# Kernel optimization log

Measured on AMD Instinct MI355X. Metric: run time of the kernel, lower is better.

Reference implementation:

```python
import jax, jax.numpy as jnp
import numpy as np

H = 1024
D = 512


def _cummax(z):
    # CumMax = cumsum(softmax(z, -1), -1)
    return jnp.cumsum(jax.nn.softmax(z, axis=-1), axis=-1)


def _onlstm_layer(x, h0, c0, W, b):
    # x: [T, M, Din]; W: [Din+H, 6H] fused (order: i, f, g, o, ftilde, itilde)
    def step(carry, xt):
        h, c = carry
        z = jnp.concatenate([xt, h], axis=-1) @ W + b  # [M, 6H]
        zi, zf, zg, zo, zft, zit = jnp.split(z, 6, axis=-1)
        f_t = jax.nn.sigmoid(zf)
        i_t = jax.nn.sigmoid(zi)
        o_t = jax.nn.sigmoid(zo)
        c_hat = jnp.tanh(zg)
        f_til = _cummax(zft)
        i_til = 1.0 - _cummax(zit)
        omega = f_til * i_til
        f_hat = f_t * omega + (f_til - omega)
        i_hat = i_t * omega + (i_til - omega)
        c = f_hat * c + i_hat * c_hat
        h = o_t * jnp.tanh(c)
        return (h, c), h

    (h_n, c_n), all_h = jax.lax.scan(step, (h0, c0), x)
    return all_h, h_n, c_n


def setup_inputs() -> dict:
    key = jax.random.key(0)
    k = jax.random.split(key, 5)
    T, M = 256, 64
    inp = {
        "input_": jax.random.normal(k[0], (T, M, D), dtype=jnp.float32),
        # fused gate weights: layer0 in = D+H, layer1 in = H+H; out = 6H
        "W0": jax.random.normal(k[1], (D + H, 6 * H), dtype=jnp.float32) / np.sqrt(D + H),
        "b0": jax.random.normal(k[2], (6 * H,), dtype=jnp.float32) * 0.01,
        "W1": jax.random.normal(k[3], (H + H, 6 * H), dtype=jnp.float32) / np.sqrt(2 * H),
        "b1": jax.random.normal(k[4], (6 * H,), dtype=jnp.float32) * 0.01,
    }
    return inp


def reference(input_, W0, b0, W1, b1):
    T, M, _ = input_.shape
    h0 = jnp.zeros((M, H), dtype=input_.dtype)
    c0 = jnp.zeros((M, H), dtype=input_.dtype)
    all_h, h0_n, c0_n = _onlstm_layer(input_, h0, c0, W0, b0)
    all_h, h1_n, c1_n = _onlstm_layer(all_h, h0, c0, W1, b1)
    h_n = jnp.stack([h0_n, h1_n])  # [num_layers, M, H]
    c_n = jnp.stack([c0_n, c1_n])
    return all_h, h_n, c_n
```

## Files before the change

kernel.cpp:

```cpp
#include <hip/hip_runtime.h>
#include <hip/hip_fp16.h>


typedef _Float16 f16;
typedef _Float16 f16x8 __attribute__((ext_vector_type(8)));
typedef _Float16 f16x2 __attribute__((ext_vector_type(2)));
typedef float f32x4 __attribute__((ext_vector_type(4)));

#define NWG 256
#define AGENT __HIP_MEMORY_SCOPE_AGENT

__device__ __forceinline__ f16x8 ld_frag(const f16* p) {
    union { unsigned long long u[2]; f16x8 v; } c;
    c.u[0] = __hip_atomic_load((const unsigned long long*)p, __ATOMIC_RELAXED, AGENT);
    c.u[1] = __hip_atomic_load(((const unsigned long long*)p) + 1, __ATOMIC_RELAXED, AGENT);
    return c.v;
}

__global__ void onlstm_pack_w(const float* __restrict__ W, f16* __restrict__ dst,
                              int nkt, int krow0) {
    int idx = blockIdx.x * blockDim.x + threadIdx.x;
    int total = 128 * 3 * nkt * 64;
    if (idx >= total) return;
    int lane = idx & 63;
    int kt = (idx >> 6) % nkt;
    int ct = ((idx >> 6) / nkt) % 3;
    int w  = (idx >> 6) / (nkt * 3);
    int cc = lane & 15;
    int gate = 2 * ct + (cc >> 3);
    int col = gate * 1024 + (w << 3) + (cc & 7);
    int krow = krow0 + kt * 32 + ((lane >> 4) << 3);
    const float* src = W + (size_t)krow * 6144 + col;
    f16x8 v;
#pragma unroll
    for (int i = 0; i < 8; ++i) v[i] = (f16)src[(size_t)i * 6144];
    *(f16x8*)(dst + (size_t)idx * 8) = v;
}

__global__ void onlstm_pack_x(const float* __restrict__ x, f16* __restrict__ dst) {
    int idx = blockIdx.x * blockDim.x + threadIdx.x;
    if (idx >= 256 * 16 * 4 * 64) return;
    int lane = idx & 63;
    int rt = (idx >> 6) & 3;
    int kt = (idx >> 8) & 15;
    int t  = idx >> 12;
    int m = rt * 16 + (lane & 15);
    int k = kt * 32 + ((lane >> 4) << 3);
    const float* src = x + ((size_t)t * 64 + m) * 512 + k;
    f16x8 v;
#pragma unroll
    for (int i = 0; i < 8; ++i) v[i] = (f16)src[i];
    *(f16x8*)(dst + (size_t)idx * 8) = v;
}

__device__ __forceinline__ float fast_sigmoid(float x) {
    return 1.0f / (1.0f + __expf(-x));
}
__device__ __forceinline__ float fast_tanh(float x) {
    return 1.0f - 2.0f / (__expf(2.0f * x) + 1.0f);
}

__global__ __launch_bounds__(256, 1) void onlstm_main(
    const f16* __restrict__ WB0, const f16* __restrict__ WB1,
    const f16* __restrict__ WS1, const f16* __restrict__ XP,
    f16* __restrict__ H0P, f16* __restrict__ H1P,
    float* __restrict__ PARTS, int* __restrict__ FLAGS,
    const float* __restrict__ b0, const float* __restrict__ b1,
    float* __restrict__ out)
{
    extern __shared__ char smem[];
    f16*   sB    = (f16*)smem;
    float* sZ    = (float*)(smem + 147456);
    float* sPfx  = (float*)(smem + 160000);
    float* sScl  = (float*)(smem + 162048);
    float* sBias = (float*)(smem + 163072);

    const int tid = threadIdx.x;
    const int wg = blockIdx.x;
    const int layer = wg >> 7;
    const int w = wg & 127;
    const int lane = tid & 63;
    const int wv = tid >> 6;
    const int rtp = wv & 1;
    const int kh = wv >> 1;
    const int j0 = w << 3;
    const int m_u = tid & 63;
    const int pr4 = tid >> 6;
    int* FA = FLAGS;
    int* FB = FLAGS + 4096;

    {
        const float4* s4 = (const float4*)(layer ? (WB1 + (size_t)w * (3 * 32 * 512))
                                                 : (WB0 + (size_t)w * (3 * 48 * 512)));
        float4* d4 = (float4*)sB;
        const int n = layer ? (3 * 32 * 64) : (3 * 48 * 64);
        for (int i = tid; i < n; i += 256) d4[i] = s4[i];
    }
    if (tid < 48) {
        int ct = tid >> 4, r = tid & 15;
        int gate = 2 * ct + (r >> 3);
        sBias[tid] = (layer ? b1 : b0)[gate * 1024 + j0 + (r & 7)];
    }
    float c0 = 0.f, c1 = 0.f;
    __syncthreads();

    for (int s = 0; s <= 256; ++s) {
        const int active = layer ? (s >= 1) : (s < 256);
        const int t = layer ? (s - 1) : s;
        const int hr = (s + 2) % 3;
        float* PARTs = PARTS + (size_t)s * 32768;

        f32x4 acc[2][3];
        if (active) {
#pragma unroll
            for (int r = 0; r < 2; ++r)
#pragma unroll
                for (int c = 0; c < 3; ++c) { f32x4 z = {0.f,0.f,0.f,0.f}; acc[r][c] = z; }

            const f16* h0r = H0P + (size_t)hr * 65536;
            const int abase = rtp * 1024 + lane * 8;

            if (layer == 0) {
                if (kh == 0) {
                    const f16* A1 = XP + (size_t)t * 32768;
#pragma unroll 8
                    for (int kt = 0; kt < 16; ++kt) {
                        const f16* ap = A1 + (size_t)kt * 2048 + abase;
                        f16x8 a0 = *(const f16x8*)ap;
                        f16x8 a1 = *(const f16x8*)(ap + 512);
#pragma unroll
                        for (int ct = 0; ct < 3; ++ct) {
                            f16x8 b = *(const f16x8*)(sB + ((size_t)(ct * 48 + kt) * 64 + lane) * 8);
                            acc[0][ct] = __builtin_amdgcn_mfma_f32_16x16x32_f16(a0, b, acc[0][ct], 0, 0, 0);
                            acc[1][ct] = __builtin_amdgcn_mfma_f32_16x16x32_f16(a1, b, acc[1][ct], 0, 0, 0);
                        }
                    }
#pragma unroll 8
                    for (int kt = 0; kt < 8; ++kt) {
                        const f16* ap = h0r + (size_t)kt * 2048 + abase;
                        f16x8 a0 = ld_frag(ap);
                        f16x8 a1 = ld_frag(ap + 512);
#pragma unroll
                        for (int ct = 0; ct < 3; ++ct) {
                            f16x8 b = *(const f16x8*)(sB + ((size_t)(ct * 48 + 16 + kt) * 64 + lane) * 8);
                            acc[0][ct] = __builtin_amdgcn_mfma_f32_16x16x32_f16(a0, b, acc[0][ct], 0, 0, 0);
                            acc[1][ct] = __builtin_amdgcn_mfma_f32_16x16x32_f16(a1, b, acc[1][ct], 0, 0, 0);
                        }
                    }
                } else {
#pragma unroll 8
                    for (int kt = 8; kt < 32; ++kt) {
                        const f16* ap = h0r + (size_t)kt * 2048 + abase;
                        f16x8 a0 = ld_frag(ap);
                        f16x8 a1 = ld_frag(ap + 512);
#pragma unroll
                        for (int ct = 0; ct < 3; ++ct) {
                            f16x8 b = *(const f16x8*)(sB + ((size_t)(ct * 48 + 16 + kt) * 64 + lane) * 8);
                            acc[0][ct] = __builtin_amdgcn_mfma_f32_16x16x32_f16(a0, b, acc[0][ct], 0, 0, 0);
                            acc[1][ct] = __builtin_amdgcn_mfma_f32_16x16x32_f16(a1, b, acc[1][ct], 0, 0, 0);
                        }
                    }
                }
            } else {
                if (kh == 0) {
                    const f16* BS = WS1 + (size_t)w * (3 * 32 * 512);
#pragma unroll 8
                    for (int kt = 0; kt < 32; ++kt) {
                        const f16* ap = h0r + (size_t)kt * 2048 + abase;
                        f16x8 a0 = ld_frag(ap);
                        f16x8 a1 = ld_frag(ap + 512);
#pragma unroll
                        for (int ct = 0; ct < 3; ++ct) {
                            f16x8 b = *(const f16x8*)(BS + ((size_t)(ct * 32 + kt) * 64 + lane) * 8);
                            acc[0][ct] = __builtin_amdgcn_mfma_f32_16x16x32_f16(a0, b, acc[0][ct], 0, 0, 0);
                            acc[1][ct] = __builtin_amdgcn_mfma_f32_16x16x32_f16(a1, b, acc[1][ct], 0, 0, 0);
                        }
                    }
                } else {
                    const f16* h1r = H1P + (size_t)(s & 1) * 65536;
#pragma unroll 8
                    for (int kt = 0; kt < 32; ++kt) {
                        const f16* ap = h1r + (size_t)kt * 2048 + abase;
                        f16x8 a0 = ld_frag(ap);
                        f16x8 a1 = ld_frag(ap + 512);
#pragma unroll
                        for (int ct = 0; ct < 3; ++ct) {
                            f16x8 b = *(const f16x8*)(sB + ((size_t)(ct * 32 + kt) * 64 + lane) * 8);
                            acc[0][ct] = __builtin_amdgcn_mfma_f32_16x16x32_f16(a0, b, acc[0][ct], 0, 0, 0);
                            acc[1][ct] = __builtin_amdgcn_mfma_f32_16x16x32_f16(a1, b, acc[1][ct], 0, 0, 0);
                        }
                    }
                }
            }
            if (kh == 1) {
                const int mq = ((lane >> 4) << 2);
                const int colb = lane & 15;
#pragma unroll
                for (int r = 0; r < 2; ++r) {
                    int mrow = rtp * 32 + r * 16 + mq;
#pragma unroll
                    for (int ct = 0; ct < 3; ++ct) {
                        int col = ct * 16 + colb;
#pragma unroll
                        for (int q = 0; q < 4; ++q)
                            sZ[(mrow + q) * 49 + col] = acc[r][ct][q];
                    }
                }
            }
        }
        __syncthreads();
        if (active && kh == 0) {
            const int mq = ((lane >> 4) << 2);
            const int colb = lane & 15;
#pragma unroll
            for (int r = 0; r < 2; ++r) {
                int mrow = rtp * 32 + r * 16 + mq;
#pragma unroll
                for (int ct = 0; ct < 3; ++ct) {
                    int col = ct * 16 + colb;
                    float bias = sBias[col];
#pragma unroll
                    for (int q = 0; q < 4; ++q) {
                        int idx = (mrow + q) * 49 + col;
                        sZ[idx] = sZ[idx] + acc[r][ct][q] + bias;
                    }
                }
            }
        }
        __syncthreads();

        if (active && tid < 128) {
            int g = tid >> 6, m = tid & 63;
            float run = 0.f;
            float* zp = sZ + m * 49 + 32 + g * 8;
#pragma unroll
            for (int jj = 0; jj < 8; ++jj) {
                float e = __expf(zp[jj]);
                run += e;
                zp[jj] = run;
            }
            __hip_atomic_store(&PARTs[((size_t)(layer * 2 + g) * 128 + w) * 64 + m], run,
                               __ATOMIC_RELAXED, AGENT);
        }

        __syncthreads();
        if (tid == 0)
            __hip_atomic_store(&FA[wg * 16], s + 1, __ATOMIC_RELAXED, AGENT);
        if (tid < 128) {
            const int* fp = &FA[(layer * 128 + tid) * 16];
            while (__hip_atomic_load(fp, __ATOMIC_RELAXED, AGENT) < s + 1) {}
        }
        __syncthreads();

        if (active) {
            int g = pr4 & 1, half = pr4 >> 1;
            const float* pp = PARTs + ((size_t)(layer * 2 + g) * 128 + half * 64) * 64 + m_u;
            float pref = 0.f, tot = 0.f;
            int wrel = w - half * 64;
#pragma unroll 32
            for (int w2 = 0; w2 < 64; ++w2) {
                float v = pp[(size_t)w2 * 64];
                tot += v;
                pref += (w2 < wrel) ? v : 0.f;
            }
            float* q = sPfx + ((size_t)(m_u * 2 + g) * 2 + half) * 2;
            q[0] = pref; q[1] = tot;
        }
        __syncthreads();
        if (active && tid < 128) {
            int g = tid >> 6, m = tid & 63;
            float* q = sPfx + (size_t)(m * 2 + g) * 4;
            sScl[m * 4 + g * 2]     = q[0] + q[2];
            sScl[m * 4 + g * 2 + 1] = 1.0f / (q[1] + q[3]);
        }
        __syncthreads();

        if (active) {
            float pf = sScl[m_u * 4 + 0], rf = sScl[m_u * 4 + 1];
            float pi = sScl[m_u * 4 + 2], ri = sScl[m_u * 4 + 3];
            int zb = m_u * 49;
            float cc[2] = {c0, c1}, hh[2];
#pragma unroll
            for (int q = 0; q < 2; ++q) {
                int jj = pr4 * 2 + q;
                float zi = sZ[zb + jj];
                float zf = sZ[zb + 8 + jj];
                float zg = sZ[zb + 16 + jj];
                float zo = sZ[zb + 24 + jj];
                float cft = sZ[zb + 32 + jj];
                float cit = sZ[zb + 40 + jj];
                float ftil = (pf + cft) * rf;
                float itil = 1.0f - (pi + cit) * ri;
                float om = ftil * itil;
                float fi = fast_sigmoid(zf);
                float ii = fast_sigmoid(zi);
                float oo = fast_sigmoid(zo);
                float ch = fast_tanh(zg);
                float fh = fi * om + (ftil - om);
                float ih = ii * om + (itil - om);
                float cn = fh * cc[q] + ih * ch;
                cc[q] = cn;
                hh[q] = oo * fast_tanh(cn);
            }
            c0 = cc[0]; c1 = cc[1];

            int jfull = j0 + pr4 * 2;
            int ktp = jfull >> 5;
            int quad = (jfull >> 3) & 3;
            int i0 = jfull & 7;
            f16* HP = layer ? (H1P + (size_t)((s + 1) & 1) * 65536)
                            : (H0P + (size_t)(s % 3) * 65536);
            union { f16x2 h; int i; } hu;
            hu.h[0] = (f16)hh[0]; hu.h[1] = (f16)hh[1];
            __hip_atomic_store(
                (int*)(HP + ((size_t)(ktp * 4 + (m_u >> 4)) * 64 + (quad * 16 + (m_u & 15))) * 8 + i0),
                hu.i, __ATOMIC_RELAXED, AGENT);

            if (layer)
                *(float2*)(out + (size_t)t * 65536 + (size_t)m_u * 1024 + jfull) = make_float2(hh[0], hh[1]);
            if (t == 255) {
                *(float2*)(out + 16777216 + (size_t)layer * 65536 + (size_t)m_u * 1024 + jfull) = make_float2(hh[0], hh[1]);
                *(float2*)(out + 16908288 + (size_t)layer * 65536 + (size_t)m_u * 1024 + jfull) = make_float2(cc[0], cc[1]);
            }
        }

        if (s < 256) {
            __syncthreads();
            if (tid == 0)
                __hip_atomic_store(&FB[wg * 16], s + 1, __ATOMIC_RELAXED, AGENT);
            if (layer == 0) {
                if (tid < 128) {
                    const int* fp = &FB[tid * 16];
                    while (__hip_atomic_load(fp, __ATOMIC_RELAXED, AGENT) < s + 1) {}
                } else {
                    const int* fp = &FA[tid * 16];
                    while (__hip_atomic_load(fp, __ATOMIC_RELAXED, AGENT) < s) {}
                }
            } else {
                const int* fp = &FB[tid * 16];
                while (__hip_atomic_load(fp, __ATOMIC_RELAXED, AGENT) < s + 1) {}
            }
            __syncthreads();
        }
    }
}

extern "C" void kernel_launch(void* const* d_in, const int* in_sizes, int n_in,
                              void* d_out, int out_size, void* d_ws, size_t ws_size,
                              hipStream_t stream) {
    const float* x  = (const float*)d_in[0];
    const float* W0 = (const float*)d_in[1];
    const float* b0 = (const float*)d_in[2];
    const float* W1 = (const float*)d_in[3];
    const float* b1 = (const float*)d_in[4];
    float* out = (float*)d_out;

    char* ws = (char*)d_ws;
    f16* WB0     = (f16*)(ws + 0);
    f16* WB1     = (f16*)(ws + 18874368);
    f16* WS1     = (f16*)(ws + 31457280);
    f16* XP      = (f16*)(ws + 44040192);
    f16* H0P     = (f16*)(ws + 60817408);
    f16* H1P     = (f16*)(ws + 61210624);
    int* FLAGS   = (int*)(ws + 61603840);
    float* PARTS = (float*)(ws + 61636608);

    hipMemsetAsync(H0P, 0, 393216, stream);
    hipMemsetAsync(H1P, 0, 262144, stream);
    hipMemsetAsync(FLAGS, 0, 32768, stream);

    {   int n = 128 * 3 * 48 * 64;
        onlstm_pack_w<<<(n + 255) / 256, 256, 0, stream>>>(W0, WB0, 48, 0); }
    {   int n = 128 * 3 * 32 * 64;
        onlstm_pack_w<<<(n + 255) / 256, 256, 0, stream>>>(W1, WB1, 32, 1024); }
    {   int n = 128 * 3 * 32 * 64;
        onlstm_pack_w<<<(n + 255) / 256, 256, 0, stream>>>(W1, WS1, 32, 0); }
    {   int n = 256 * 16 * 4 * 64;
        onlstm_pack_x<<<(n + 255) / 256, 256, 0, stream>>>(x, XP); }

    const int smem_bytes = 163328;
    hipFuncSetAttribute((const void*)onlstm_main,
                        hipFuncAttributeMaxDynamicSharedMemorySize, smem_bytes);
    onlstm_main<<<NWG, 256, smem_bytes, stream>>>(WB0, WB1, WS1, XP, H0P, H1P,
                                                  PARTS, FLAGS, b0, b1, out);
}
```

Measured before the change: 4.691 ms.

## Software-pipeline recurrent h loads and deepen the layer-0 h ring buffer

Restructures the recurrent GEMM loops to prefetch eight k-tiles of h fragments into registers ahead of the MFMAs, overlapping the coherent atomic loads with compute. It also grows the layer-0 hidden-state ring from three to four slots and relaxes the layer-0 wait on layer-1 progress by one step, giving the two pipelined layers more slack. This costs more registers and a larger workspace buffer, and it changes the cross-layer synchronisation contract, which has to stay correct.

```diff
diff --git a/kernel.cpp b/kernel.cpp
--- a/kernel.cpp
+++ b/kernel.cpp
@@ -9,6 +9,7 @@
 
 #define NWG 256
 #define AGENT __HIP_MEMORY_SCOPE_AGENT
+#define MFMA16 __builtin_amdgcn_mfma_f32_16x16x32_f16
 
 __device__ __forceinline__ f16x8 ld_frag(const f16* p) {
     union { unsigned long long u[2]; f16x8 v; } c;
@@ -107,7 +108,7 @@
     for (int s = 0; s <= 256; ++s) {
         const int active = layer ? (s >= 1) : (s < 256);
         const int t = layer ? (s - 1) : s;
-        const int hr = (s + 2) % 3;
+        const int hr = (s + 3) & 3;
         float* PARTs = PARTS + (size_t)s * 32768;
 
         f32x4 acc[2][3];
@@ -131,63 +132,109 @@
 #pragma unroll
                         for (int ct = 0; ct < 3; ++ct) {
                             f16x8 b = *(const f16x8*)(sB + ((size_t)(ct * 48 + kt) * 64 + lane) * 8);
-                            acc[0][ct] = __builtin_amdgcn_mfma_f32_16x16x32_f16(a0, b, acc[0][ct], 0, 0, 0);
-                            acc[1][ct] = __builtin_amdgcn_mfma_f32_16x16x32_f16(a1, b, acc[1][ct], 0, 0, 0);
+                            acc[0][ct] = MFMA16(a0, b, acc[0][ct], 0, 0, 0);
+                            acc[1][ct] = MFMA16(a1, b, acc[1][ct], 0, 0, 0);
                         }
                     }
-#pragma unroll 8
-                    for (int kt = 0; kt < 8; ++kt) {
-                        const f16* ap = h0r + (size_t)kt * 2048 + abase;
-                        f16x8 a0 = ld_frag(ap);
-                        f16x8 a1 = ld_frag(ap + 512);
+                    f16x8 p0[8], p1[8];
+#pragma unroll
+                    for (int k = 0; k < 8; ++k) {
+                        const f16* ap = h0r + (size_t)k * 2048 + abase;
+                        p0[k] = ld_frag(ap);
+                        p1[k] = ld_frag(ap + 512);
+                    }
+#pragma unroll
+                    for (int k = 0; k < 8; ++k) {
 #pragma unroll
                         for (int ct = 0; ct < 3; ++ct) {
-                            f16x8 b = *(const f16x8*)(sB + ((size_t)(ct * 48 + 16 + kt) * 64 + lane) * 8);
-                            acc[0][ct] = __builtin_amdgcn_mfma_f32_16x16x32_f16(a0, b, acc[0][ct], 0, 0, 0);
-                            acc[1][ct] = __builtin_amdgcn_mfma_f32_16x16x32_f16(a1, b, acc[1][ct], 0, 0, 0);
+                            f16x8 b = *(const f16x8*)(sB + ((size_t)(ct * 48 + 16 + k) * 64 + lane) * 8);
+                            acc[0][ct] = MFMA16(p0[k], b, acc[0][ct], 0, 0, 0);
+                            acc[1][ct] = MFMA16(p1[k], b, acc[1][ct], 0, 0, 0);
                         }
                     }
                 } else {
-#pragma unroll 8
-                    for (int kt = 8; kt < 32; ++kt) {
-                        const f16* ap = h0r + (size_t)kt * 2048 + abase;
-                        f16x8 a0 = ld_frag(ap);
-                        f16x8 a1 = ld_frag(ap + 512);
-#pragma unroll
-                        for (int ct = 0; ct < 3; ++ct) {
-                            f16x8 b = *(const f16x8*)(sB + ((size_t)(ct * 48 + 16 + kt) * 64 + lane) * 8);
-                            acc[0][ct] = __builtin_amdgcn_mfma_f32_16x16x32_f16(a0, b, acc[0][ct], 0, 0, 0);
-                            acc[1][ct] = __builtin_amdgcn_mfma_f32_16x16x32_f16(a1, b, acc[1][ct], 0, 0, 0);
+                    f16x8 p0[8], p1[8];
+#pragma unroll
+                    for (int k = 0; k < 8; ++k) {
+                        const f16* ap = h0r + (size_t)(8 + k) * 2048 + abase;
+                        p0[k] = ld_frag(ap);
+                        p1[k] = ld_frag(ap + 512);
+                    }
+#pragma unroll
+                    for (int c = 0; c < 3; ++c) {
+#pragma unroll
+                        for (int k = 0; k < 8; ++k) {
+                            const int kt = 8 + c * 8 + k;
+                            f16x8 a0 = p0[k], a1 = p1[k];
+                            if (c < 2) {
+                                const f16* ap = h0r + (size_t)(kt + 8) * 2048 + abase;
+                                p0[k] = ld_frag(ap);
+                                p1[k] = ld_frag(ap + 512);
+                            }
+#pragma unroll
+                            for (int ct = 0; ct < 3; ++ct) {
+                                f16x8 b = *(const f16x8*)(sB + ((size_t)(ct * 48 + 16 + kt) * 64 + lane) * 8);
+                                acc[0][ct] = MFMA16(a0, b, acc[0][ct], 0, 0, 0);
+                                acc[1][ct] = MFMA16(a1, b, acc[1][ct], 0, 0, 0);
+                            }
                         }
                     }
                 }
             } else {
                 if (kh == 0) {
                     const f16* BS = WS1 + (size_t)w * (3 * 32 * 512);
-#pragma unroll 8
-                    for (int kt = 0; kt < 32; ++kt) {
-                        const f16* ap = h0r + (size_t)kt * 2048 + abase;
-                        f16x8 a0 = ld_frag(ap);
-                        f16x8 a1 = ld_frag(ap + 512);
-#pragma unroll
-                        for (int ct = 0; ct < 3; ++ct) {
-                            f16x8 b = *(const f16x8*)(BS + ((size_t)(ct * 32 + kt) * 64 + lane) * 8);
-                            acc[0][ct] = __builtin_amdgcn_mfma_f32_16x16x32_f16(a0, b, acc[0][ct], 0, 0, 0);
-                            acc[1][ct] = __builtin_amdgcn_mfma_f32_16x16x32_f16(a1, b, acc[1][ct], 0, 0, 0);
+                    f16x8 p0[8], p1[8];
+#pragma unroll
+                    for (int k = 0; k < 8; ++k) {
+                        const f16* ap = h0r + (size_t)k * 2048 + abase;
+                        p0[k] = ld_frag(ap);
+                        p1[k] = ld_frag(ap + 512);
+                    }
+#pragma unroll
+                    for (int c = 0; c < 4; ++c) {
+#pragma unroll
+                        for (int k = 0; k < 8; ++k) {
+                            const int kt = c * 8 + k;
+                            f16x8 a0 = p0[k], a1 = p1[k];
+                            if (c < 3) {
+                                const f16* ap = h0r + (size_t)(kt + 8) * 2048 + abase;
+                                p0[k] = ld_frag(ap);
+                                p1[k] = ld_frag(ap + 512);
+                            }
+#pragma unroll
+                            for (int ct = 0; ct < 3; ++ct) {
+                                f16x8 b = *(const f16x8*)(BS + ((size_t)(ct * 32 + kt) * 64 + lane) * 8);
+                                acc[0][ct] = MFMA16(a0, b, acc[0][ct], 0, 0, 0);
+                                acc[1][ct] = MFMA16(a1, b, acc[1][ct], 0, 0, 0);
+                            }
                         }
                     }
                 } else {
                     const f16* h1r = H1P + (size_t)(s & 1) * 65536;
-#pragma unroll 8
-                    for (int kt = 0; kt < 32; ++kt) {
-                        const f16* ap = h1r + (size_t)kt * 2048 + abase;
-                        f16x8 a0 = ld_frag(ap);
-                        f16x8 a1 = ld_frag(ap + 512);
-#pragma unroll
-                        for (int ct = 0; ct < 3; ++ct) {
-                            f16x8 b = *(const f16x8*)(sB + ((size_t)(ct * 32 + kt) * 64 + lane) * 8);
-                            acc[0][ct] = __builtin_amdgcn_mfma_f32_16x16x32_f16(a0, b, acc[0][ct], 0, 0, 0);
-                            acc[1][ct] = __builtin_amdgcn_mfma_f32_16x16x32_f16(a1, b, acc[1][ct], 0, 0, 0);
+                    f16x8 p0[8], p1[8];
+#pragma unroll
+                    for (int k = 0; k < 8; ++k) {
+                        const f16* ap = h1r + (size_t)k * 2048 + abase;
+                        p0[k] = ld_frag(ap);
+                        p1[k] = ld_frag(ap + 512);
+                    }
+#pragma unroll
+                    for (int c = 0; c < 4; ++c) {
+#pragma unroll
+                        for (int k = 0; k < 8; ++k) {
+                            const int kt = c * 8 + k;
+                            f16x8 a0 = p0[k], a1 = p1[k];
+                            if (c < 3) {
+                                const f16* ap = h1r + (size_t)(kt + 8) * 2048 + abase;
+                                p0[k] = ld_frag(ap);
+                                p1[k] = ld_frag(ap + 512);
+                            }
+#pragma unroll
+                            for (int ct = 0; ct < 3; ++ct) {
+                                f16x8 b = *(const f16x8*)(sB + ((size_t)(ct * 32 + kt) * 64 + lane) * 8);
+                                acc[0][ct] = MFMA16(a0, b, acc[0][ct], 0, 0, 0);
+                                acc[1][ct] = MFMA16(a1, b, acc[1][ct], 0, 0, 0);
+                            }
                         }
                     }
                 }
@@ -309,7 +356,7 @@
             int quad = (jfull >> 3) & 3;
             int i0 = jfull & 7;
             f16* HP = layer ? (H1P + (size_t)((s + 1) & 1) * 65536)
-                            : (H0P + (size_t)(s % 3) * 65536);
+                            : (H0P + (size_t)(s & 3) * 65536);
             union { f16x2 h; int i; } hu;
             hu.h[0] = (f16)hh[0]; hu.h[1] = (f16)hh[1];
             __hip_atomic_store(
@@ -334,7 +381,7 @@
                     while (__hip_atomic_load(fp, __ATOMIC_RELAXED, AGENT) < s + 1) {}
                 } else {
                     const int* fp = &FA[tid * 16];
-                    while (__hip_atomic_load(fp, __ATOMIC_RELAXED, AGENT) < s) {}
+                    while (__hip_atomic_load(fp, __ATOMIC_RELAXED, AGENT) < s - 1) {}
                 }
             } else {
                 const int* fp = &FB[tid * 16];
@@ -361,11 +408,11 @@
     f16* WS1     = (f16*)(ws + 31457280);
     f16* XP      = (f16*)(ws + 44040192);
     f16* H0P     = (f16*)(ws + 60817408);
-    f16* H1P     = (f16*)(ws + 61210624);
+    f16* H1P     = (f16*)(ws + 61341696);
     int* FLAGS   = (int*)(ws + 61603840);
     float* PARTS = (float*)(ws + 61636608);
 
-    hipMemsetAsync(H0P, 0, 393216, stream);
+    hipMemsetAsync(H0P, 0, 524288, stream);
     hipMemsetAsync(H1P, 0, 262144, stream);
     hipMemsetAsync(FLAGS, 0, 32768, stream);
 
```

New measurement: 8.846 ms. 88.6% more time.

## Use per-timestep hidden-state buffers to drop WAR flag waits and atomic loads

Applied to the files above, without the earlier changes.

When the workspace is large enough, each timestep's hidden state gets its own buffer instead of a rotating triple or double buffer. Because buffers are never overwritten, the layer-1-to-layer-0 back-pressure spin wait is removed, and hidden fragments are read with plain vector loads instead of relaxed atomic loads. The cost is a much larger workspace footprint, and the plain loads may be served by stale cache lines, since freshness rests on the first write to each address. The old rotating-buffer path is kept as a fallback when the workspace is small.

```diff
diff --git a/kernel.cpp b/kernel.cpp
--- a/kernel.cpp
+++ b/kernel.cpp
@@ -9,12 +9,19 @@
 
 #define NWG 256
 #define AGENT __HIP_MEMORY_SCOPE_AGENT
+#define MFMA16 __builtin_amdgcn_mfma_f32_16x16x32_f16
 
 __device__ __forceinline__ f16x8 ld_frag(const f16* p) {
     union { unsigned long long u[2]; f16x8 v; } c;
     c.u[0] = __hip_atomic_load((const unsigned long long*)p, __ATOMIC_RELAXED, AGENT);
     c.u[1] = __hip_atomic_load(((const unsigned long long*)p) + 1, __ATOMIC_RELAXED, AGENT);
     return c.v;
+}
+
+template<int FRESH>
+__device__ __forceinline__ f16x8 ld_h(const f16* p) {
+    if constexpr (FRESH) return *(const f16x8*)p;
+    else return ld_frag(p);
 }
 
 __global__ void onlstm_pack_w(const float* __restrict__ W, f16* __restrict__ dst,
@@ -60,6 +67,7 @@
     return 1.0f - 2.0f / (__expf(2.0f * x) + 1.0f);
 }
 
+template<int FRESH>
 __global__ __launch_bounds__(256, 1) void onlstm_main(
     const f16* __restrict__ WB0, const f16* __restrict__ WB1,
     const f16* __restrict__ WS1, const f16* __restrict__ XP,
@@ -107,7 +115,7 @@
     for (int s = 0; s <= 256; ++s) {
         const int active = layer ? (s >= 1) : (s < 256);
         const int t = layer ? (s - 1) : s;
-        const int hr = (s + 2) % 3;
+        const int hr = FRESH ? s : ((s + 2) % 3);
         float* PARTs = PARTS + (size_t)s * 32768;
 
         f32x4 acc[2][3];
@@ -131,33 +139,33 @@
 #pragma unroll
                         for (int ct = 0; ct < 3; ++ct) {
                             f16x8 b = *(const f16x8*)(sB + ((size_t)(ct * 48 + kt) * 64 + lane) * 8);
-                            acc[0][ct] = __builtin_amdgcn_mfma_f32_16x16x32_f16(a0, b, acc[0][ct], 0, 0, 0);
-                            acc[1][ct] = __builtin_amdgcn_mfma_f32_16x16x32_f16(a1, b, acc[1][ct], 0, 0, 0);
+                            acc[0][ct] = MFMA16(a0, b, acc[0][ct], 0, 0, 0);
+                            acc[1][ct] = MFMA16(a1, b, acc[1][ct], 0, 0, 0);
                         }
                     }
 #pragma unroll 8
                     for (int kt = 0; kt < 8; ++kt) {
                         const f16* ap = h0r + (size_t)kt * 2048 + abase;
-                        f16x8 a0 = ld_frag(ap);
-                        f16x8 a1 = ld_frag(ap + 512);
+                        f16x8 a0 = ld_h<FRESH>(ap);
+                        f16x8 a1 = ld_h<FRESH>(ap + 512);
 #pragma unroll
                         for (int ct = 0; ct < 3; ++ct) {
                             f16x8 b = *(const f16x8*)(sB + ((size_t)(ct * 48 + 16 + kt) * 64 + lane) * 8);
-                            acc[0][ct] = __builtin_amdgcn_mfma_f32_16x16x32_f16(a0, b, acc[0][ct], 0, 0, 0);
-                            acc[1][ct] = __builtin_amdgcn_mfma_f32_16x16x32_f16(a1, b, acc[1][ct], 0, 0, 0);
+                            acc[0][ct] = MFMA16(a0, b, acc[0][ct], 0, 0, 0);
+                            acc[1][ct] = MFMA16(a1, b, acc[1][ct], 0, 0, 0);
                         }
                     }
                 } else {
 #pragma unroll 8
                     for (int kt = 8; kt < 32; ++kt) {
                         const f16* ap = h0r + (size_t)kt * 2048 + abase;
-                        f16x8 a0 = ld_frag(ap);
-                        f16x8 a1 = ld_frag(ap + 512);
+                        f16x8 a0 = ld_h<FRESH>(ap);
+                        f16x8 a1 = ld_h<FRESH>(ap + 512);
 #pragma unroll
                         for (int ct = 0; ct < 3; ++ct) {
                             f16x8 b = *(const f16x8*)(sB + ((size_t)(ct * 48 + 16 + kt) * 64 + lane) * 8);
-                            acc[0][ct] = __builtin_amdgcn_mfma_f32_16x16x32_f16(a0, b, acc[0][ct], 0, 0, 0);
-                            acc[1][ct] = __builtin_amdgcn_mfma_f32_16x16x32_f16(a1, b, acc[1][ct], 0, 0, 0);
+                            acc[0][ct] = MFMA16(a0, b, acc[0][ct], 0, 0, 0);
+                            acc[1][ct] = MFMA16(a1, b, acc[1][ct], 0, 0, 0);
                         }
                     }
                 }
@@ -167,27 +175,27 @@
 #pragma unroll 8
                     for (int kt = 0; kt < 32; ++kt) {
                         const f16* ap = h0r + (size_t)kt * 2048 + abase;
-                        f16x8 a0 = ld_frag(ap);
-                        f16x8 a1 = ld_frag(ap + 512);
+                        f16x8 a0 = ld_h<FRESH>(ap);
+                        f16x8 a1 = ld_h<FRESH>(ap + 512);
 #pragma unroll
                         for (int ct = 0; ct < 3; ++ct) {
                             f16x8 b = *(const f16x8*)(BS + ((size_t)(ct * 32 + kt) * 64 + lane) * 8);
-                            acc[0][ct] = __builtin_amdgcn_mfma_f32_16x16x32_f16(a0, b, acc[0][ct], 0, 0, 0);
-                            acc[1][ct] = __builtin_amdgcn_mfma_f32_16x16x32_f16(a1, b, acc[1][ct], 0, 0, 0);
+                            acc[0][ct] = MFMA16(a0, b, acc[0][ct], 0, 0, 0);
+                            acc[1][ct] = MFMA16(a1, b, acc[1][ct], 0, 0, 0);
                         }
                     }
                 } else {
-                    const f16* h1r = H1P + (size_t)(s & 1) * 65536;
+                    const f16* h1r = H1P + (size_t)(FRESH ? (s - 1) : (s & 1)) * 65536;
 #pragma unroll 8
                     for (int kt = 0; kt < 32; ++kt) {
                         const f16* ap = h1r + (size_t)kt * 2048 + abase;
-                        f16x8 a0 = ld_frag(ap);
-                        f16x8 a1 = ld_frag(ap + 512);
+                        f16x8 a0 = ld_h<FRESH>(ap);
+                        f16x8 a1 = ld_h<FRESH>(ap + 512);
 #pragma unroll
                         for (int ct = 0; ct < 3; ++ct) {
                             f16x8 b = *(const f16x8*)(sB + ((size_t)(ct * 32 + kt) * 64 + lane) * 8);
-                            acc[0][ct] = __builtin_amdgcn_mfma_f32_16x16x32_f16(a0, b, acc[0][ct], 0, 0, 0);
-                            acc[1][ct] = __builtin_amdgcn_mfma_f32_16x16x32_f16(a1, b, acc[1][ct], 0, 0, 0);
+                            acc[0][ct] = MFMA16(a0, b, acc[0][ct], 0, 0, 0);
+                            acc[1][ct] = MFMA16(a1, b, acc[1][ct], 0, 0, 0);
                         }
                     }
                 }
@@ -308,8 +316,8 @@
             int ktp = jfull >> 5;
             int quad = (jfull >> 3) & 3;
             int i0 = jfull & 7;
-            f16* HP = layer ? (H1P + (size_t)((s + 1) & 1) * 65536)
-                            : (H0P + (size_t)(s % 3) * 65536);
+            f16* HP = layer ? (H1P + (size_t)(FRESH ? s : ((s + 1) & 1)) * 65536)
+                            : (H0P + (size_t)(FRESH ? (s + 1) : (s % 3)) * 65536);
             union { f16x2 h; int i; } hu;
             hu.h[0] = (f16)hh[0]; hu.h[1] = (f16)hh[1];
             __hip_atomic_store(
@@ -332,7 +340,7 @@
                 if (tid < 128) {
                     const int* fp = &FB[tid * 16];
                     while (__hip_atomic_load(fp, __ATOMIC_RELAXED, AGENT) < s + 1) {}
-                } else {
+                } else if constexpr (!FRESH) {
                     const int* fp = &FA[tid * 16];
                     while (__hip_atomic_load(fp, __ATOMIC_RELAXED, AGENT) < s) {}
                 }
@@ -356,17 +364,29 @@
     float* out = (float*)d_out;
 
     char* ws = (char*)d_ws;
-    f16* WB0     = (f16*)(ws + 0);
-    f16* WB1     = (f16*)(ws + 18874368);
-    f16* WS1     = (f16*)(ws + 31457280);
-    f16* XP      = (f16*)(ws + 44040192);
-    f16* H0P     = (f16*)(ws + 60817408);
-    f16* H1P     = (f16*)(ws + 61210624);
-    int* FLAGS   = (int*)(ws + 61603840);
-    float* PARTS = (float*)(ws + 61636608);
-
-    hipMemsetAsync(H0P, 0, 393216, stream);
-    hipMemsetAsync(H1P, 0, 262144, stream);
+    f16* WB0 = (f16*)(ws + 0);
+    f16* WB1 = (f16*)(ws + 18874368);
+    f16* WS1 = (f16*)(ws + 31457280);
+    f16* XP  = (f16*)(ws + 44040192);
+
+    const int fresh = (ws_size >= (size_t)161906688) ? 1 : 0;
+
+    f16* H0P; f16* H1P; float* PARTS; int* FLAGS;
+    if (fresh) {
+        H0P   = (f16*)(ws + 60817408);
+        H1P   = (f16*)(ws + 94502912);
+        PARTS = (float*)(ws + 128188416);
+        FLAGS = (int*)(ws + 161873920);
+        hipMemsetAsync(H0P, 0, 131072, stream);
+        hipMemsetAsync(H1P, 0, 131072, stream);
+    } else {
+        H0P   = (f16*)(ws + 60817408);
+        H1P   = (f16*)(ws + 61210624);
+        FLAGS = (int*)(ws + 61603840);
+        PARTS = (float*)(ws + 61636608);
+        hipMemsetAsync(H0P, 0, 393216, stream);
+        hipMemsetAsync(H1P, 0, 262144, stream);
+    }
     hipMemsetAsync(FLAGS, 0, 32768, stream);
 
     {   int n = 128 * 3 * 48 * 64;
@@ -379,8 +399,15 @@
         onlstm_pack_x<<<(n + 255) / 256, 256, 0, stream>>>(x, XP); }
 
     const int smem_bytes = 163328;
-    hipFuncSetAttribute((const void*)onlstm_main,
-                        hipFuncAttributeMaxDynamicSharedMemorySize, smem_bytes);
-    onlstm_main<<<NWG, 256, smem_bytes, stream>>>(WB0, WB1, WS1, XP, H0P, H1P,
-                                                  PARTS, FLAGS, b0, b1, out);
-}
+    if (fresh) {
+        hipFuncSetAttribute((const void*)onlstm_main<1>,
+                            hipFuncAttributeMaxDynamicSharedMemorySize, smem_bytes);
+        onlstm_main<1><<<NWG, 256, smem_bytes, stream>>>(WB0, WB1, WS1, XP, H0P, H1P,
+                                                         PARTS, FLAGS, b0, b1, out);
+    } else {
+        hipFuncSetAttribute((const void*)onlstm_main<0>,
+                            hipFuncAttributeMaxDynamicSharedMemorySize, smem_bytes);
+        onlstm_main<0><<<NWG, 256, smem_bytes, stream>>>(WB0, WB1, WS1, XP, H0P, H1P,
+                                                         PARTS, FLAGS, b0, b1, out);
+    }
+}
```

Result: slower. 6.339 ms (+35.1%).
